# Optimization experiments

Hardware: AMD Instinct MI355X
Metric: run time of the kernel (lower is better)

The kernel has to match this reference:

```python
import jax, jax.numpy as jnp
import numpy as np

B, L = 8, 2500
VOCAB = 50000 + 2
E = 100          # dims[0], embed size
D = 128          # dims[1], conv filters
Y = 8921         # number of ICD9 labels
K = 9            # conv kernel size
PAD = K // 2


def setup_inputs() -> dict:
    key = jax.random.key(0)
    ks = jax.random.split(key, 8)
    x = jax.random.randint(ks[0], (B, L), 0, 50000)                      # token ids
    target = jax.random.uniform(ks[1], (B, Y), dtype=jnp.float32)        # soft binary targets
    emb_table = jax.random.normal(ks[2], (VOCAB, E), dtype=jnp.float32) * 0.1
    emb_table = emb_table.at[0].set(0.0)                                 # padding_idx=0
    # xavier-uniform-ish scales
    conv_w = jax.random.uniform(ks[3], (D, E, K), dtype=jnp.float32,
                                minval=-1.0, maxval=1.0) * np.sqrt(6.0 / (E * K + D * K))
    conv_b = jnp.zeros((D,), dtype=jnp.float32)
    U = jax.random.uniform(ks[4], (Y, D), dtype=jnp.float32,
                           minval=-1.0, maxval=1.0) * np.sqrt(6.0 / (Y + D))
    final_w = jax.random.uniform(ks[5], (Y, D), dtype=jnp.float32,
                                 minval=-1.0, maxval=1.0) * np.sqrt(6.0 / (Y + D))
    final_b = jnp.zeros((Y,), dtype=jnp.float32)
    return {"x": x, "target": target, "emb_table": emb_table,
            "conv_w": conv_w, "conv_b": conv_b, "U": U,
            "final_w": final_w, "final_b": final_b}


def _bce_with_logits(logits, target):
    # mean(max(z,0) - z*t + log(1+exp(-|z|)))
    return jnp.mean(jnp.maximum(logits, 0.0) - logits * target
                    + jnp.log1p(jnp.exp(-jnp.abs(logits))))


def reference(x, target, emb_table, conv_w, conv_b, U, final_w, final_b):
    e = emb_table[x]                                  # [B, L, E]  (dropout inactive at eval)
    # Conv1d over sequence, 'same' padding; conv_w is torch layout (Cout, Cin, K)
    h = jax.lax.conv_general_dilated(
        e, conv_w, window_strides=(1,), padding=[(PAD, PAD)],
        dimension_numbers=("NWC", "OIW", "NWC")) + conv_b
    h = jnp.tanh(h)                                   # [B, L, D]
    # Label-wise attention: scores [B, Y, L], softmax over sequence dim
    scores = jnp.einsum("yd,bld->byl", U, h)
    alpha = jax.nn.softmax(scores, axis=2)            # [B, Y, L]
    m = jnp.einsum("byl,bld->byd", alpha, h)          # [B, Y, D]
    logits = jnp.einsum("yd,byd->by", final_w, m) + final_b   # [B, Y]
    loss = _bce_with_logits(logits, target)
    yhat = jax.nn.sigmoid(logits)
    return yhat, loss, alpha
```

## Files before the change

kernel.cpp:

```cpp
#include <hip/hip_runtime.h>
#include <math.h>

#define B 8
#define LSEQ 2500
#define EDIM 100
#define DDIM 128
#define YLAB 8921
#define KW 9
#define BYTOT (B*YLAB)
#define LP 2560
#define NLBS 20
#define NYB 70
#define NPB 140

typedef __attribute__((ext_vector_type(8))) short bf16x8;
typedef __attribute__((ext_vector_type(8))) unsigned short u16x8;
typedef __attribute__((ext_vector_type(4))) float f32x4;

__device__ __forceinline__ ushort f2bf(float f){
    union { float f; unsigned u; } v; v.f = f;
    unsigned r = v.u + 0x7FFFu + ((v.u >> 16) & 1u);
    return (ushort)(r >> 16);
}
__device__ __forceinline__ float bf2f(ushort u){
    union { unsigned u; float f; } v; v.u = ((unsigned)u) << 16;
    return v.f;
}

#define OFF_HB 0
#define OFF_HT 1310720
#define OFF_UB 2621440
#define OFF_PS 3192384
#define OFF_RI 4619744
#define OFF_LG 4691112
#define OFF_LSP 4762480
#define OFF_WT 4762608

#define NP1 (DDIM*EDIM*KW)
#define NP2 (YLAB*DDIM)
#define NP3 (B*DDIM*(LP-LSEQ))
#define NP4 (B*(LP-LSEQ)*DDIM)
__global__ __launch_bounds__(256) void k_prep(const float* __restrict__ w, const float* __restrict__ U,
                                              float* __restrict__ wT, ushort* __restrict__ Ub,
                                              ushort* __restrict__ hT, ushort* __restrict__ hb){
    int i = blockIdx.x * 256 + threadIdx.x;
    if (i < NP1) {
        int k = i % KW, e = (i / KW) % EDIM, d = i / (KW * EDIM);
        wT[(k * EDIM + e) * DDIM + d] = w[i];
    }
    int i2 = i - NP1;
    if (i2 >= 0 && i2 < NP2) Ub[i2] = f2bf(U[i2]);
    int i3 = i - NP1 - NP2;
    if (i3 >= 0 && i3 < NP3) {
        int c = i3 % (LP - LSEQ), bd = i3 / (LP - LSEQ);
        hT[(size_t)bd * LP + LSEQ + c] = 0;
    }
    int i4 = i - NP1 - NP2 - NP3;
    if (i4 >= 0 && i4 < NP4) {
        int b = i4 / ((LP - LSEQ) * DDIM);
        int r = i4 % ((LP - LSEQ) * DDIM);
        int l = LSEQ + r / DDIM, d = r % DDIM;
        hb[((size_t)b * LP + l) * DDIM + d] = 0;
    }
}

#define CTL 20
__global__ __launch_bounds__(256) void k_conv(const int* __restrict__ x, const float* __restrict__ emb,
                                              const float* __restrict__ wT, const float* __restrict__ bias,
                                              ushort* __restrict__ hb, ushort* __restrict__ hT) {
    __shared__ float se[EDIM * 32];
    __shared__ ushort hstage[DDIM][CTL + 2];
    int blk = blockIdx.x;
    int b = blk / (LSEQ / CTL);
    int l0 = (blk % (LSEQ / CTL)) * CTL;
    int tid = threadIdx.x;
    for (int i = tid; i < (CTL + 8) * EDIM; i += 256) {
        int row = i / EDIM, e = i - row * EDIM;
        int l = l0 + row - 4;
        float v = 0.f;
        if (l >= 0 && l < LSEQ) {
            int tok = x[b * LSEQ + l];
            v = emb[(size_t)tok * EDIM + e];
        }
        se[e * 32 + row] = v;
    }
    __syncthreads();
    int d = tid & 127;
    int g = tid >> 7;
    float bv = bias[d];
    float acc[10];
#pragma unroll
    for (int li = 0; li < 10; li++) acc[li] = bv;
    for (int e = 0; e < EDIM; e++) {
        float r[20];
#pragma unroll
        for (int t2 = 0; t2 < 10; t2++) {
            float2 rr = *(const float2*)&se[e * 32 + g * 10 + 2 * t2];
            r[2 * t2] = rr.x; r[2 * t2 + 1] = rr.y;
        }
#pragma unroll
        for (int k = 0; k < KW; k++) {
            float wv = wT[(k * EDIM + e) * DDIM + d];
#pragma unroll
            for (int li = 0; li < 10; li++) acc[li] += r[li + k] * wv;
        }
    }
#pragma unroll
    for (int li = 0; li < 10; li++) {
        int l = l0 + g * 10 + li;
        ushort u = f2bf(tanhf(acc[li]));
        hb[((size_t)b * LP + l) * DDIM + d] = u;
        hstage[d][g * 10 + li] = u;
    }
    __syncthreads();
    int d2 = tid >> 1, half = tid & 1;
    size_t base = ((size_t)b * DDIM + d2) * LP + l0 + half * 10;
#pragma unroll
    for (int q = 0; q < 10; q++) hT[base + q] = hstage[d2][half * 10 + q];
}

__global__ __launch_bounds__(256) void k_sums(const ushort* __restrict__ hb, const ushort* __restrict__ Ub,
                                              float* __restrict__ psum) {
    int wg = blockIdx.x;
    int b = wg & 7;
    int r = wg >> 3;
    int lblk = r % NLBS, yblk = r / NLBS;
    int l0 = lblk * 128, y0 = yblk * 128;
    int tid = threadIdx.x, w = tid >> 6, lane = tid & 63, g = lane >> 4, ln = lane & 15;
    int h = w >> 1, lh = w & 1;
    int y0w = y0 + h * 64;
    bf16x8 zf = {0, 0, 0, 0, 0, 0, 0, 0};
    bf16x8 au[4][4];
    bool vya[4];
#pragma unroll
    for (int yf = 0; yf < 4; yf++) {
        int ya = y0w + yf * 16 + ln;
        vya[yf] = ya < YLAB;
        const ushort* Ap = Ub + (size_t)(vya[yf] ? ya : 0) * DDIM + g * 8;
#pragma unroll
        for (int kk = 0; kk < 4; kk++) au[yf][kk] = vya[yf] ? *(const bf16x8*)(Ap + kk * 32) : zf;
    }
    f32x4 zero4 = {0.f, 0.f, 0.f, 0.f};
    const ushort* hbB = hb + (size_t)b * LP * DDIM;
    float ts[4][4] = {};
#pragma unroll
    for (int lt = 0; lt < 2; lt++) {
        int lw = l0 + (lt * 2 + lh) * 32;
        f32x4 acc[4][2];
#pragma unroll
        for (int yf = 0; yf < 4; yf++) { acc[yf][0] = zero4; acc[yf][1] = zero4; }
#pragma unroll
        for (int kk = 0; kk < 4; kk++) {
            bf16x8 bv0 = *(const bf16x8*)(hbB + (size_t)(lw + ln) * DDIM + kk * 32 + g * 8);
            bf16x8 bv1 = *(const bf16x8*)(hbB + (size_t)(lw + 16 + ln) * DDIM + kk * 32 + g * 8);
#pragma unroll
            for (int yf = 0; yf < 4; yf++) {
                acc[yf][0] = __builtin_amdgcn_mfma_f32_16x16x32_bf16(au[yf][kk], bv0, acc[yf][0], 0, 0, 0);
                acc[yf][1] = __builtin_amdgcn_mfma_f32_16x16x32_bf16(au[yf][kk], bv1, acc[yf][1], 0, 0, 0);
            }
        }
#pragma unroll
        for (int yf = 0; yf < 4; yf++)
#pragma unroll
            for (int fl = 0; fl < 2; fl++)
#pragma unroll
                for (int j = 0; j < 4; j++) {
                    int y = y0w + yf * 16 + g * 4 + j;
                    int l = lw + fl * 16 + ln;
                    bool v = (y < YLAB) && (l < LSEQ);
                    ts[yf][j] += v ? __expf(acc[yf][fl][j]) : 0.f;
                }
    }
#pragma unroll
    for (int yf = 0; yf < 4; yf++)
#pragma unroll
        for (int j = 0; j < 4; j++) {
            float t = ts[yf][j];
            t += __shfl_xor(t, 1, 64); t += __shfl_xor(t, 2, 64);
            t += __shfl_xor(t, 4, 64); t += __shfl_xor(t, 8, 64);
            ts[yf][j] = t;
        }
    __shared__ float psl[2][128];
    if (ln == 0) {
#pragma unroll
        for (int yf = 0; yf < 4; yf++)
#pragma unroll
            for (int j = 0; j < 4; j++)
                psl[lh][h * 64 + yf * 16 + g * 4 + j] = ts[yf][j];
    }
    __syncthreads();
    if (tid < 128) {
        int y = y0 + tid;
        if (y < YLAB) psum[(size_t)lblk * BYTOT + b * YLAB + y] = psl[0][tid] + psl[1][tid];
    }
}

__global__ __launch_bounds__(256) void k_rinv(const float* __restrict__ psum, float* __restrict__ rinv) {
    int i = blockIdx.x * 256 + threadIdx.x;
    if (i >= BYTOT) return;
    float s = 0.f;
#pragma unroll
    for (int j = 0; j < NLBS; j++) s += psum[(size_t)j * BYTOT + i];
    rinv[i] = 1.f / s;
}

__global__ __launch_bounds__(256) void k_pool(const ushort* __restrict__ hb, const ushort* __restrict__ hT,
                                              const ushort* __restrict__ Ub, const float* __restrict__ rinv,
                                              const float* __restrict__ fw, const float* __restrict__ fb,
                                              float* __restrict__ alpha, float* __restrict__ yhat,
                                              float* __restrict__ logits) {
    __shared__ ushort hbs[32 * 128];
    __shared__ ushort hts[128 * 40];
    __shared__ ushort et[4][16 * 44];
    int wg = blockIdx.x;
    int b = wg & 7;
    int y0 = (wg >> 3) * 64;
    int tid = threadIdx.x, w = tid >> 6, lane = tid & 63, g = lane >> 4, ln = lane & 15;
    int y0w = y0 + w * 16;
    bf16x8 zf = {0, 0, 0, 0, 0, 0, 0, 0};
    int ya = y0w + ln;
    bool vya = ya < YLAB;
    const ushort* Ap = Ub + (size_t)(vya ? ya : 0) * DDIM + g * 8;
    bf16x8 au[4];
#pragma unroll
    for (int kk = 0; kk < 4; kk++) au[kk] = vya ? *(const bf16x8*)(Ap + kk * 32) : zf;
    float rvl = vya ? rinv[b * YLAB + ya] : 0.f;
    f32x4 zero4 = {0.f, 0.f, 0.f, 0.f};
    f32x4 accm[8];
#pragma unroll
    for (int fd = 0; fd < 8; fd++) accm[fd] = zero4;

    int s0 = tid, s1 = tid + 256;
    const ushort* hbB = hb + (size_t)b * LP * DDIM;
    const ushort* htB = hT + (size_t)b * DDIM * LP;
    int l_a = s0 >> 4, sg_a = s0 & 15, l_b = s1 >> 4, sg_b = s1 & 15;
    int d_a = s0 >> 2, q_a = s0 & 3, d_b = s1 >> 2, q_b = s1 & 3;
    int wsg_a = sg_a ^ (l_a & 7), wsg_b = sg_b ^ (l_b & 7);
    u16x8 rhb0, rhb1, rht0, rht1;
    rhb0 = *(const u16x8*)(hbB + (size_t)l_a * DDIM + sg_a * 8);
    rhb1 = *(const u16x8*)(hbB + (size_t)l_b * DDIM + sg_b * 8);
    rht0 = *(const u16x8*)(htB + (size_t)d_a * LP + q_a * 8);
    rht1 = *(const u16x8*)(htB + (size_t)d_b * LP + q_b * 8);

    float* aB = alpha + (size_t)b * YLAB * LSEQ;

    for (int l0 = 0; l0 < LP; l0 += 32) {
        *(u16x8*)&hbs[l_a * DDIM + wsg_a * 8] = rhb0;
        *(u16x8*)&hbs[l_b * DDIM + wsg_b * 8] = rhb1;
        *(u16x8*)&hts[d_a * 40 + q_a * 8] = rht0;
        *(u16x8*)&hts[d_b * 40 + q_b * 8] = rht1;
        __syncthreads();
        if (l0 + 32 < LP) {
            int ln0 = l0 + 32;
            rhb0 = *(const u16x8*)(hbB + (size_t)(ln0 + l_a) * DDIM + sg_a * 8);
            rhb1 = *(const u16x8*)(hbB + (size_t)(ln0 + l_b) * DDIM + sg_b * 8);
            rht0 = *(const u16x8*)(htB + (size_t)d_a * LP + ln0 + q_a * 8);
            rht1 = *(const u16x8*)(htB + (size_t)d_b * LP + ln0 + q_b * 8);
        }
        f32x4 sc[2];
        sc[0] = zero4; sc[1] = zero4;
#pragma unroll
        for (int kk = 0; kk < 4; kk++)
#pragma unroll
            for (int fl = 0; fl < 2; fl++) {
                int lrow = fl * 16 + ln;
                int slotr = (kk * 4 + g) ^ (lrow & 7);
                bf16x8 bv = *(const bf16x8*)&hbs[lrow * DDIM + slotr * 8];
                sc[fl] = __builtin_amdgcn_mfma_f32_16x16x32_bf16(bv, au[kk], sc[fl], 0, 0, 0);
            }
#pragma unroll
        for (int fl = 0; fl < 2; fl++) {
            float an0 = __expf(sc[fl][0]) * rvl;
            float an1 = __expf(sc[fl][1]) * rvl;
            float an2 = __expf(sc[fl][2]) * rvl;
            float an3 = __expf(sc[fl][3]) * rvl;
            unsigned long long pk =
                (unsigned long long)f2bf(an0) | ((unsigned long long)f2bf(an1) << 16) |
                ((unsigned long long)f2bf(an2) << 32) | ((unsigned long long)f2bf(an3) << 48);
            *(unsigned long long*)&et[w][ln * 44 + fl * 16 + g * 4] = pk;
        }
        bf16x8 af = *(const bf16x8*)&et[w][ln * 44 + g * 8];
#pragma unroll
        for (int fd = 0; fd < 8; fd++) {
            bf16x8 bt = *(const bf16x8*)&hts[(fd * 16 + ln) * 40 + g * 8];
            accm[fd] = __builtin_amdgcn_mfma_f32_16x16x32_bf16(af, bt, accm[fd], 0, 0, 0);
        }
        if (l0 + 32 <= LSEQ) {
#pragma unroll
            for (int i = 0; i < 8; i++) {
                int r = i * 2 + (lane >> 5);
                int c = lane & 31;
                int y = y0w + r;
                if (y < YLAB) aB[(size_t)y * LSEQ + l0 + c] = bf2f(et[w][r * 44 + c]);
            }
        } else if (l0 < LSEQ) {
#pragma unroll
            for (int i = 0; i < 8; i++) {
                int r = i * 2 + (lane >> 5);
                int c = lane & 31;
                int y = y0w + r;
                int l = l0 + c;
                if (y < YLAB && l < LSEQ) aB[(size_t)y * LSEQ + l] = bf2f(et[w][r * 44 + c]);
            }
        }
        __syncthreads();
    }
    float lp[4] = {0.f, 0.f, 0.f, 0.f};
#pragma unroll
    for (int j = 0; j < 4; j++) {
        int yr = y0w + g * 4 + j;
        bool vr = yr < YLAB;
#pragma unroll
        for (int fd = 0; fd < 8; fd++) {
            float fwv = vr ? fw[(size_t)yr * DDIM + fd * 16 + ln] : 0.f;
            lp[j] += accm[fd][j] * fwv;
        }
    }
#pragma unroll
    for (int j = 0; j < 4; j++) {
        float t = lp[j];
        t += __shfl_xor(t, 1, 64); t += __shfl_xor(t, 2, 64);
        t += __shfl_xor(t, 4, 64); t += __shfl_xor(t, 8, 64);
        lp[j] = t;
    }
    if (ln == 0) {
#pragma unroll
        for (int j = 0; j < 4; j++) {
            int yr = y0w + g * 4 + j;
            if (yr < YLAB) {
                float lg = lp[j] + fb[yr];
                int idx = b * YLAB + yr;
                logits[idx] = lg;
                yhat[idx] = 1.f / (1.f + expf(-lg));
            }
        }
    }
}

__global__ __launch_bounds__(256) void k_loss1(const float* __restrict__ logits, const float* __restrict__ target,
                                               float* __restrict__ partials) {
    int tid = threadIdx.x;
    int base = blockIdx.x * 1024;
    float sum = 0.f;
#pragma unroll
    for (int q = 0; q < 4; q++) {
        int i = base + q * 256 + tid;
        if (i < BYTOT) {
            float z = logits[i], t = target[i];
            sum += fmaxf(z, 0.f) - z * t + log1pf(expf(-fabsf(z)));
        }
    }
    for (int o = 32; o > 0; o >>= 1) sum += __shfl_down(sum, o, 64);
    __shared__ float red[4];
    if ((tid & 63) == 0) red[tid >> 6] = sum;
    __syncthreads();
    if (tid == 0) partials[blockIdx.x] = red[0] + red[1] + red[2] + red[3];
}

__global__ __launch_bounds__(128) void k_loss2(const float* __restrict__ partials, float* __restrict__ out_loss) {
    int tid = threadIdx.x;
    float s = (tid < 70) ? partials[tid] : 0.f;
    for (int o = 32; o > 0; o >>= 1) s += __shfl_down(s, o, 64);
    __shared__ float red[2];
    if ((tid & 63) == 0) red[tid >> 6] = s;
    __syncthreads();
    if (tid == 0) out_loss[0] = (red[0] + red[1]) / (float)BYTOT;
}

extern "C" void kernel_launch(void* const* d_in, const int* in_sizes, int n_in,
                              void* d_out, int out_size, void* d_ws, size_t ws_size,
                              hipStream_t stream) {
    const int* x = (const int*)d_in[0];
    const float* target = (const float*)d_in[1];
    const float* emb = (const float*)d_in[2];
    const float* conv_w = (const float*)d_in[3];
    const float* conv_b = (const float*)d_in[4];
    const float* U = (const float*)d_in[5];
    const float* fw = (const float*)d_in[6];
    const float* fb = (const float*)d_in[7];

    float* out = (float*)d_out;
    float* yhat = out;
    float* loss = out + BYTOT;
    float* alpha = out + BYTOT + 1;

    float* ws = (float*)d_ws;
    ushort* hb = (ushort*)(ws + OFF_HB);
    ushort* hT = (ushort*)(ws + OFF_HT);
    ushort* Ub = (ushort*)(ws + OFF_UB);
    float* psum = ws + OFF_PS;
    float* rinv = ws + OFF_RI;
    float* logits = ws + OFF_LG;
    float* lpart = ws + OFF_LSP;
    float* wT = ws + OFF_WT;

    k_prep<<<(NP1 + NP2 + NP3 + NP4 + 255) / 256, 256, 0, stream>>>(conv_w, U, wT, Ub, hT, hb);
    k_conv<<<B * (LSEQ / CTL), 256, 0, stream>>>(x, emb, wT, conv_b, hb, hT);
    k_sums<<<NYB * NLBS * B, 256, 0, stream>>>(hb, Ub, psum);
    k_rinv<<<(BYTOT + 255) / 256, 256, 0, stream>>>(psum, rinv);
    k_pool<<<NPB * B, 256, 0, stream>>>(hb, hT, Ub, rinv, fw, fb, alpha, yhat, logits);
    k_loss1<<<70, 256, 0, stream>>>(logits, target, lpart);
    k_loss2<<<1, 128, 0, stream>>>(lpart, loss);
}
```

Before: 634.3 us.

## Materialize unnormalized exp scores in k_sums and reuse them in k_pool

k_sums now writes the bf16 exp(score) values to a workspace buffer of shape [B*Y, LP] alongside the partial sums. k_pool no longer recomputes the U·h scores. It streams these stored exponentials, scales them by the reciprocal sum to produce alpha, and applies the normalization to the logits after the weighted pooling. This removes the second score GEMM and the exp work, and drops the LDS staging and barriers. The cost is writing and re-reading a roughly 365 MB bf16 intermediate, so the kernel leans much harder on memory bandwidth. Alpha is also now rounded from the unnormalized bf16 exponential and then scaled.

```diff
diff --git a/kernel.cpp b/kernel.cpp
--- a/kernel.cpp
+++ b/kernel.cpp
@@ -12,9 +12,9 @@
 #define NLBS 20
 #define NYB 70
 #define NPB 140
+#define LPOOL 2528
 
 typedef __attribute__((ext_vector_type(8))) short bf16x8;
-typedef __attribute__((ext_vector_type(8))) unsigned short u16x8;
 typedef __attribute__((ext_vector_type(4))) float f32x4;
 
 __device__ __forceinline__ ushort f2bf(float f){
@@ -35,6 +35,7 @@
 #define OFF_LG 4691112
 #define OFF_LSP 4762480
 #define OFF_WT 4762608
+#define OFF_EB 4877808
 
 #define NP1 (DDIM*EDIM*KW)
 #define NP2 (YLAB*DDIM)
@@ -120,78 +121,74 @@
 }
 
 __global__ __launch_bounds__(256) void k_sums(const ushort* __restrict__ hb, const ushort* __restrict__ Ub,
-                                              float* __restrict__ psum) {
+                                              float* __restrict__ psum, ushort* __restrict__ ebuf) {
     int wg = blockIdx.x;
     int b = wg & 7;
     int r = wg >> 3;
     int lblk = r % NLBS, yblk = r / NLBS;
     int l0 = lblk * 128, y0 = yblk * 128;
     int tid = threadIdx.x, w = tid >> 6, lane = tid & 63, g = lane >> 4, ln = lane & 15;
-    int h = w >> 1, lh = w & 1;
-    int y0w = y0 + h * 64;
+    int y0w = y0 + w * 32;
     bf16x8 zf = {0, 0, 0, 0, 0, 0, 0, 0};
-    bf16x8 au[4][4];
-    bool vya[4];
-#pragma unroll
-    for (int yf = 0; yf < 4; yf++) {
-        int ya = y0w + yf * 16 + ln;
-        vya[yf] = ya < YLAB;
-        const ushort* Ap = Ub + (size_t)(vya[yf] ? ya : 0) * DDIM + g * 8;
-#pragma unroll
-        for (int kk = 0; kk < 4; kk++) au[yf][kk] = vya[yf] ? *(const bf16x8*)(Ap + kk * 32) : zf;
-    }
+    bf16x8 au[2][4];
+    bool vya[2];
+    int yv[2];
+#pragma unroll
+    for (int yg = 0; yg < 2; yg++) {
+        int y = y0w + yg * 16 + ln;
+        vya[yg] = y < YLAB;
+        yv[yg] = vya[yg] ? y : 0;
+        const ushort* Ap = Ub + (size_t)yv[yg] * DDIM + g * 8;
+#pragma unroll
+        for (int kk = 0; kk < 4; kk++) au[yg][kk] = vya[yg] ? *(const bf16x8*)(Ap + kk * 32) : zf;
+    }
+    const ushort* hbB = hb + (size_t)b * LP * DDIM;
     f32x4 zero4 = {0.f, 0.f, 0.f, 0.f};
-    const ushort* hbB = hb + (size_t)b * LP * DDIM;
-    float ts[4][4] = {};
-#pragma unroll
-    for (int lt = 0; lt < 2; lt++) {
-        int lw = l0 + (lt * 2 + lh) * 32;
-        f32x4 acc[4][2];
-#pragma unroll
-        for (int yf = 0; yf < 4; yf++) { acc[yf][0] = zero4; acc[yf][1] = zero4; }
-#pragma unroll
-        for (int kk = 0; kk < 4; kk++) {
-            bf16x8 bv0 = *(const bf16x8*)(hbB + (size_t)(lw + ln) * DDIM + kk * 32 + g * 8);
-            bf16x8 bv1 = *(const bf16x8*)(hbB + (size_t)(lw + 16 + ln) * DDIM + kk * 32 + g * 8);
-#pragma unroll
-            for (int yf = 0; yf < 4; yf++) {
-                acc[yf][0] = __builtin_amdgcn_mfma_f32_16x16x32_bf16(au[yf][kk], bv0, acc[yf][0], 0, 0, 0);
-                acc[yf][1] = __builtin_amdgcn_mfma_f32_16x16x32_bf16(au[yf][kk], bv1, acc[yf][1], 0, 0, 0);
+    float ts[2] = {0.f, 0.f};
+#pragma unroll
+    for (int lt = 0; lt < 4; lt++) {
+        int lw = l0 + lt * 32;
+        bf16x8 a[2][4];
+#pragma unroll
+        for (int fl = 0; fl < 2; fl++)
+#pragma unroll
+            for (int kk = 0; kk < 4; kk++)
+                a[fl][kk] = *(const bf16x8*)(hbB + (size_t)(lw + fl * 16 + ln) * DDIM + kk * 32 + g * 8);
+        f32x4 sc[2][2];
+        sc[0][0] = zero4; sc[0][1] = zero4; sc[1][0] = zero4; sc[1][1] = zero4;
+#pragma unroll
+        for (int kk = 0; kk < 4; kk++)
+#pragma unroll
+            for (int fl = 0; fl < 2; fl++) {
+                sc[0][fl] = __builtin_amdgcn_mfma_f32_16x16x32_bf16(a[fl][kk], au[0][kk], sc[0][fl], 0, 0, 0);
+                sc[1][fl] = __builtin_amdgcn_mfma_f32_16x16x32_bf16(a[fl][kk], au[1][kk], sc[1][fl], 0, 0, 0);
             }
-        }
-#pragma unroll
-        for (int yf = 0; yf < 4; yf++)
-#pragma unroll
-            for (int fl = 0; fl < 2; fl++)
-#pragma unroll
-                for (int j = 0; j < 4; j++) {
-                    int y = y0w + yf * 16 + g * 4 + j;
-                    int l = lw + fl * 16 + ln;
-                    bool v = (y < YLAB) && (l < LSEQ);
-                    ts[yf][j] += v ? __expf(acc[yf][fl][j]) : 0.f;
-                }
-    }
-#pragma unroll
-    for (int yf = 0; yf < 4; yf++)
-#pragma unroll
-        for (int j = 0; j < 4; j++) {
-            float t = ts[yf][j];
-            t += __shfl_xor(t, 1, 64); t += __shfl_xor(t, 2, 64);
-            t += __shfl_xor(t, 4, 64); t += __shfl_xor(t, 8, 64);
-            ts[yf][j] = t;
-        }
-    __shared__ float psl[2][128];
-    if (ln == 0) {
-#pragma unroll
-        for (int yf = 0; yf < 4; yf++)
-#pragma unroll
-            for (int j = 0; j < 4; j++)
-                psl[lh][h * 64 + yf * 16 + g * 4 + j] = ts[yf][j];
-    }
-    __syncthreads();
-    if (tid < 128) {
-        int y = y0 + tid;
-        if (y < YLAB) psum[(size_t)lblk * BYTOT + b * YLAB + y] = psl[0][tid] + psl[1][tid];
+#pragma unroll
+        for (int yg = 0; yg < 2; yg++) {
+            size_t ebrow = (size_t)(b * YLAB + yv[yg]) * LP;
+#pragma unroll
+            for (int fl = 0; fl < 2; fl++) {
+                float e0, e1, e2, e3;
+                int lb = lw + fl * 16 + g * 4;
+                e0 = (lb + 0 < LSEQ) ? __expf(sc[yg][fl][0]) : 0.f;
+                e1 = (lb + 1 < LSEQ) ? __expf(sc[yg][fl][1]) : 0.f;
+                e2 = (lb + 2 < LSEQ) ? __expf(sc[yg][fl][2]) : 0.f;
+                e3 = (lb + 3 < LSEQ) ? __expf(sc[yg][fl][3]) : 0.f;
+                ts[yg] += (e0 + e1) + (e2 + e3);
+                unsigned long long pk =
+                    (unsigned long long)f2bf(e0) | ((unsigned long long)f2bf(e1) << 16) |
+                    ((unsigned long long)f2bf(e2) << 32) | ((unsigned long long)f2bf(e3) << 48);
+                if (vya[yg]) *(unsigned long long*)&ebuf[ebrow + lb] = pk;
+            }
+        }
+    }
+#pragma unroll
+    for (int yg = 0; yg < 2; yg++) {
+        float t = ts[yg];
+        t += __shfl_xor(t, 16, 64);
+        t += __shfl_xor(t, 32, 64);
+        if (g == 0 && vya[yg])
+            psum[(size_t)lblk * BYTOT + b * YLAB + y0w + yg * 16 + ln] = t;
     }
 }
 
@@ -204,106 +201,56 @@
     rinv[i] = 1.f / s;
 }
 
-__global__ __launch_bounds__(256) void k_pool(const ushort* __restrict__ hb, const ushort* __restrict__ hT,
-                                              const ushort* __restrict__ Ub, const float* __restrict__ rinv,
-                                              const float* __restrict__ fw, const float* __restrict__ fb,
-                                              float* __restrict__ alpha, float* __restrict__ yhat,
-                                              float* __restrict__ logits) {
-    __shared__ ushort hbs[32 * 128];
-    __shared__ ushort hts[128 * 40];
-    __shared__ ushort et[4][16 * 44];
+__global__ __launch_bounds__(256) void k_pool(const ushort* __restrict__ ebuf, const ushort* __restrict__ hT,
+                                              const float* __restrict__ rinv, const float* __restrict__ fw,
+                                              const float* __restrict__ fb, float* __restrict__ alpha,
+                                              float* __restrict__ yhat, float* __restrict__ logits) {
     int wg = blockIdx.x;
     int b = wg & 7;
     int y0 = (wg >> 3) * 64;
     int tid = threadIdx.x, w = tid >> 6, lane = tid & 63, g = lane >> 4, ln = lane & 15;
     int y0w = y0 + w * 16;
-    bf16x8 zf = {0, 0, 0, 0, 0, 0, 0, 0};
     int ya = y0w + ln;
     bool vya = ya < YLAB;
-    const ushort* Ap = Ub + (size_t)(vya ? ya : 0) * DDIM + g * 8;
-    bf16x8 au[4];
-#pragma unroll
-    for (int kk = 0; kk < 4; kk++) au[kk] = vya ? *(const bf16x8*)(Ap + kk * 32) : zf;
+    int yc = vya ? ya : 0;
     float rvl = vya ? rinv[b * YLAB + ya] : 0.f;
+    const ushort* eR = ebuf + (size_t)(b * YLAB + yc) * LP + g * 8;
+    const ushort* htB = hT + (size_t)b * DDIM * LP + g * 8;
+    float* aRow = alpha + (size_t)(b * YLAB + yc) * LSEQ;
+    bf16x8 zf = {0, 0, 0, 0, 0, 0, 0, 0};
     f32x4 zero4 = {0.f, 0.f, 0.f, 0.f};
     f32x4 accm[8];
 #pragma unroll
     for (int fd = 0; fd < 8; fd++) accm[fd] = zero4;
 
-    int s0 = tid, s1 = tid + 256;
-    const ushort* hbB = hb + (size_t)b * LP * DDIM;
-    const ushort* htB = hT + (size_t)b * DDIM * LP;
-    int l_a = s0 >> 4, sg_a = s0 & 15, l_b = s1 >> 4, sg_b = s1 & 15;
-    int d_a = s0 >> 2, q_a = s0 & 3, d_b = s1 >> 2, q_b = s1 & 3;
-    int wsg_a = sg_a ^ (l_a & 7), wsg_b = sg_b ^ (l_b & 7);
-    u16x8 rhb0, rhb1, rht0, rht1;
-    rhb0 = *(const u16x8*)(hbB + (size_t)l_a * DDIM + sg_a * 8);
-    rhb1 = *(const u16x8*)(hbB + (size_t)l_b * DDIM + sg_b * 8);
-    rht0 = *(const u16x8*)(htB + (size_t)d_a * LP + q_a * 8);
-    rht1 = *(const u16x8*)(htB + (size_t)d_b * LP + q_b * 8);
-
-    float* aB = alpha + (size_t)b * YLAB * LSEQ;
-
-    for (int l0 = 0; l0 < LP; l0 += 32) {
-        *(u16x8*)&hbs[l_a * DDIM + wsg_a * 8] = rhb0;
-        *(u16x8*)&hbs[l_b * DDIM + wsg_b * 8] = rhb1;
-        *(u16x8*)&hts[d_a * 40 + q_a * 8] = rht0;
-        *(u16x8*)&hts[d_b * 40 + q_b * 8] = rht1;
-        __syncthreads();
-        if (l0 + 32 < LP) {
-            int ln0 = l0 + 32;
-            rhb0 = *(const u16x8*)(hbB + (size_t)(ln0 + l_a) * DDIM + sg_a * 8);
-            rhb1 = *(const u16x8*)(hbB + (size_t)(ln0 + l_b) * DDIM + sg_b * 8);
-            rht0 = *(const u16x8*)(htB + (size_t)d_a * LP + ln0 + q_a * 8);
-            rht1 = *(const u16x8*)(htB + (size_t)d_b * LP + ln0 + q_b * 8);
-        }
-        f32x4 sc[2];
-        sc[0] = zero4; sc[1] = zero4;
-#pragma unroll
-        for (int kk = 0; kk < 4; kk++)
-#pragma unroll
-            for (int fl = 0; fl < 2; fl++) {
-                int lrow = fl * 16 + ln;
-                int slotr = (kk * 4 + g) ^ (lrow & 7);
-                bf16x8 bv = *(const bf16x8*)&hbs[lrow * DDIM + slotr * 8];
-                sc[fl] = __builtin_amdgcn_mfma_f32_16x16x32_bf16(bv, au[kk], sc[fl], 0, 0, 0);
+    for (int l0 = 0; l0 < LPOOL; l0 += 32) {
+        bf16x8 ar = *(const bf16x8*)(eR + l0);
+        bf16x8 af = vya ? ar : zf;
+#pragma unroll
+        for (int fd = 0; fd < 8; fd++) {
+            bf16x8 bt = *(const bf16x8*)(htB + (size_t)(fd * 16 + ln) * LP + l0);
+            accm[fd] = __builtin_amdgcn_mfma_f32_16x16x32_bf16(af, bt, accm[fd], 0, 0, 0);
+        }
+        if (vya) {
+            float f[8];
+#pragma unroll
+            for (int q = 0; q < 8; q++) f[q] = bf2f((ushort)ar[q]) * rvl;
+            int lb = l0 + g * 8;
+            if (lb + 8 <= LSEQ) {
+                *(float4*)&aRow[lb] = make_float4(f[0], f[1], f[2], f[3]);
+                *(float4*)&aRow[lb + 4] = make_float4(f[4], f[5], f[6], f[7]);
+            } else {
+#pragma unroll
+                for (int q = 0; q < 8; q++)
+                    if (lb + q < LSEQ) aRow[lb + q] = f[q];
             }
-#pragma unroll
-        for (int fl = 0; fl < 2; fl++) {
-            float an0 = __expf(sc[fl][0]) * rvl;
-            float an1 = __expf(sc[fl][1]) * rvl;
-            float an2 = __expf(sc[fl][2]) * rvl;
-            float an3 = __expf(sc[fl][3]) * rvl;
-            unsigned long long pk =
-                (unsigned long long)f2bf(an0) | ((unsigned long long)f2bf(an1) << 16) |
-                ((unsigned long long)f2bf(an2) << 32) | ((unsigned long long)f2bf(an3) << 48);
-            *(unsigned long long*)&et[w][ln * 44 + fl * 16 + g * 4] = pk;
-        }
-        bf16x8 af = *(const bf16x8*)&et[w][ln * 44 + g * 8];
-#pragma unroll
-        for (int fd = 0; fd < 8; fd++) {
-            bf16x8 bt = *(const bf16x8*)&hts[(fd * 16 + ln) * 40 + g * 8];
-            accm[fd] = __builtin_amdgcn_mfma_f32_16x16x32_bf16(af, bt, accm[fd], 0, 0, 0);
-        }
-        if (l0 + 32 <= LSEQ) {
-#pragma unroll
-            for (int i = 0; i < 8; i++) {
-                int r = i * 2 + (lane >> 5);
-                int c = lane & 31;
-                int y = y0w + r;
-                if (y < YLAB) aB[(size_t)y * LSEQ + l0 + c] = bf2f(et[w][r * 44 + c]);
-            }
-        } else if (l0 < LSEQ) {
-#pragma unroll
-            for (int i = 0; i < 8; i++) {
-                int r = i * 2 + (lane >> 5);
-                int c = lane & 31;
-                int y = y0w + r;
-                int l = l0 + c;
-                if (y < YLAB && l < LSEQ) aB[(size_t)y * LSEQ + l] = bf2f(et[w][r * 44 + c]);
-            }
-        }
-        __syncthreads();
+        }
+    }
+    float rin4[4];
+#pragma unroll
+    for (int j = 0; j < 4; j++) {
+        int yr = y0w + g * 4 + j;
+        rin4[j] = (yr < YLAB) ? rinv[b * YLAB + yr] : 0.f;
     }
     float lp[4] = {0.f, 0.f, 0.f, 0.f};
 #pragma unroll
@@ -321,7 +268,7 @@
         float t = lp[j];
         t += __shfl_xor(t, 1, 64); t += __shfl_xor(t, 2, 64);
         t += __shfl_xor(t, 4, 64); t += __shfl_xor(t, 8, 64);
-        lp[j] = t;
+        lp[j] = t * rin4[j];
     }
     if (ln == 0) {
 #pragma unroll
@@ -393,12 +340,13 @@
     float* logits = ws + OFF_LG;
     float* lpart = ws + OFF_LSP;
     float* wT = ws + OFF_WT;
+    ushort* ebuf = (ushort*)(ws + OFF_EB);
 
     k_prep<<<(NP1 + NP2 + NP3 + NP4 + 255) / 256, 256, 0, stream>>>(conv_w, U, wT, Ub, hT, hb);
     k_conv<<<B * (LSEQ / CTL), 256, 0, stream>>>(x, emb, wT, conv_b, hb, hT);
-    k_sums<<<NYB * NLBS * B, 256, 0, stream>>>(hb, Ub, psum);
+    k_sums<<<NYB * NLBS * B, 256, 0, stream>>>(hb, Ub, psum, ebuf);
     k_rinv<<<(BYTOT + 255) / 256, 256, 0, stream>>>(psum, rinv);
-    k_pool<<<NPB * B, 256, 0, stream>>>(hb, hT, Ub, rinv, fw, fb, alpha, yhat, logits);
+    k_pool<<<NPB * B, 256, 0, stream>>>(ebuf, hT, rinv, fw, fb, alpha, yhat, logits);
     k_loss1<<<70, 256, 0, stream>>>(logits, target, lpart);
     k_loss2<<<1, 128, 0, stream>>>(lpart, loss);
 }
```

Result: slower. 1.049 ms (+65.4%).

## Fold softmax normalizer reduction into pool kernel and retile k_sums per-wave

Applied to the files above, without the earlier changes.

Removes the separate k_rinv launch. Each pool workgroup now sums the partial exp-sums for its 64 labels into shared memory and reads the reciprocal after the first barrier. k_sums is retiled so each wave owns 32 labels across all 128 positions, with h as the MFMA A operand, which leaves the label sums in lane-local registers. That cuts the shuffle, shared-memory and barrier reduction down to two cross-group shuffles. The cost is redundant psum reads across workgroups that share a label block, and a different register and load pattern in k_sums.

```diff
diff --git a/kernel.cpp b/kernel.cpp
--- a/kernel.cpp
+++ b/kernel.cpp
@@ -31,7 +31,6 @@
 #define OFF_HT 1310720
 #define OFF_UB 2621440
 #define OFF_PS 3192384
-#define OFF_RI 4619744
 #define OFF_LG 4691112
 #define OFF_LSP 4762480
 #define OFF_WT 4762608
@@ -127,91 +126,68 @@
     int lblk = r % NLBS, yblk = r / NLBS;
     int l0 = lblk * 128, y0 = yblk * 128;
     int tid = threadIdx.x, w = tid >> 6, lane = tid & 63, g = lane >> 4, ln = lane & 15;
-    int h = w >> 1, lh = w & 1;
-    int y0w = y0 + h * 64;
+    int y0w = y0 + w * 32;
     bf16x8 zf = {0, 0, 0, 0, 0, 0, 0, 0};
-    bf16x8 au[4][4];
-    bool vya[4];
-#pragma unroll
-    for (int yf = 0; yf < 4; yf++) {
-        int ya = y0w + yf * 16 + ln;
-        vya[yf] = ya < YLAB;
-        const ushort* Ap = Ub + (size_t)(vya[yf] ? ya : 0) * DDIM + g * 8;
-#pragma unroll
-        for (int kk = 0; kk < 4; kk++) au[yf][kk] = vya[yf] ? *(const bf16x8*)(Ap + kk * 32) : zf;
-    }
+    bf16x8 au[2][4];
+    bool vya[2];
+#pragma unroll
+    for (int yg = 0; yg < 2; yg++) {
+        int y = y0w + yg * 16 + ln;
+        vya[yg] = y < YLAB;
+        const ushort* Ap = Ub + (size_t)(vya[yg] ? y : 0) * DDIM + g * 8;
+#pragma unroll
+        for (int kk = 0; kk < 4; kk++) au[yg][kk] = vya[yg] ? *(const bf16x8*)(Ap + kk * 32) : zf;
+    }
+    const ushort* hbB = hb + (size_t)b * LP * DDIM;
     f32x4 zero4 = {0.f, 0.f, 0.f, 0.f};
-    const ushort* hbB = hb + (size_t)b * LP * DDIM;
-    float ts[4][4] = {};
-#pragma unroll
-    for (int lt = 0; lt < 2; lt++) {
-        int lw = l0 + (lt * 2 + lh) * 32;
-        f32x4 acc[4][2];
-#pragma unroll
-        for (int yf = 0; yf < 4; yf++) { acc[yf][0] = zero4; acc[yf][1] = zero4; }
-#pragma unroll
-        for (int kk = 0; kk < 4; kk++) {
-            bf16x8 bv0 = *(const bf16x8*)(hbB + (size_t)(lw + ln) * DDIM + kk * 32 + g * 8);
-            bf16x8 bv1 = *(const bf16x8*)(hbB + (size_t)(lw + 16 + ln) * DDIM + kk * 32 + g * 8);
-#pragma unroll
-            for (int yf = 0; yf < 4; yf++) {
-                acc[yf][0] = __builtin_amdgcn_mfma_f32_16x16x32_bf16(au[yf][kk], bv0, acc[yf][0], 0, 0, 0);
-                acc[yf][1] = __builtin_amdgcn_mfma_f32_16x16x32_bf16(au[yf][kk], bv1, acc[yf][1], 0, 0, 0);
-            }
-        }
-#pragma unroll
-        for (int yf = 0; yf < 4; yf++)
-#pragma unroll
-            for (int fl = 0; fl < 2; fl++)
-#pragma unroll
-                for (int j = 0; j < 4; j++) {
-                    int y = y0w + yf * 16 + g * 4 + j;
-                    int l = lw + fl * 16 + ln;
-                    bool v = (y < YLAB) && (l < LSEQ);
-                    ts[yf][j] += v ? __expf(acc[yf][fl][j]) : 0.f;
-                }
-    }
-#pragma unroll
-    for (int yf = 0; yf < 4; yf++)
-#pragma unroll
-        for (int j = 0; j < 4; j++) {
-            float t = ts[yf][j];
-            t += __shfl_xor(t, 1, 64); t += __shfl_xor(t, 2, 64);
-            t += __shfl_xor(t, 4, 64); t += __shfl_xor(t, 8, 64);
-            ts[yf][j] = t;
-        }
-    __shared__ float psl[2][128];
-    if (ln == 0) {
-#pragma unroll
-        for (int yf = 0; yf < 4; yf++)
-#pragma unroll
-            for (int j = 0; j < 4; j++)
-                psl[lh][h * 64 + yf * 16 + g * 4 + j] = ts[yf][j];
-    }
-    __syncthreads();
-    if (tid < 128) {
-        int y = y0 + tid;
-        if (y < YLAB) psum[(size_t)lblk * BYTOT + b * YLAB + y] = psl[0][tid] + psl[1][tid];
-    }
-}
-
-__global__ __launch_bounds__(256) void k_rinv(const float* __restrict__ psum, float* __restrict__ rinv) {
-    int i = blockIdx.x * 256 + threadIdx.x;
-    if (i >= BYTOT) return;
-    float s = 0.f;
-#pragma unroll
-    for (int j = 0; j < NLBS; j++) s += psum[(size_t)j * BYTOT + i];
-    rinv[i] = 1.f / s;
+    float ts[2] = {0.f, 0.f};
+#pragma unroll
+    for (int lt = 0; lt < 4; lt++) {
+        int lw = l0 + lt * 32;
+        bf16x8 a[2][4];
+#pragma unroll
+        for (int fl = 0; fl < 2; fl++)
+#pragma unroll
+            for (int kk = 0; kk < 4; kk++)
+                a[fl][kk] = *(const bf16x8*)(hbB + (size_t)(lw + fl * 16 + ln) * DDIM + kk * 32 + g * 8);
+        f32x4 sc[2][2];
+        sc[0][0] = zero4; sc[0][1] = zero4; sc[1][0] = zero4; sc[1][1] = zero4;
+#pragma unroll
+        for (int kk = 0; kk < 4; kk++)
+#pragma unroll
+            for (int fl = 0; fl < 2; fl++) {
+                sc[0][fl] = __builtin_amdgcn_mfma_f32_16x16x32_bf16(a[fl][kk], au[0][kk], sc[0][fl], 0, 0, 0);
+                sc[1][fl] = __builtin_amdgcn_mfma_f32_16x16x32_bf16(a[fl][kk], au[1][kk], sc[1][fl], 0, 0, 0);
+            }
+#pragma unroll
+        for (int yg = 0; yg < 2; yg++)
+#pragma unroll
+            for (int fl = 0; fl < 2; fl++) {
+                int lb = lw + fl * 16 + g * 4;
+#pragma unroll
+                for (int j = 0; j < 4; j++)
+                    ts[yg] += (lb + j < LSEQ) ? __expf(sc[yg][fl][j]) : 0.f;
+            }
+    }
+#pragma unroll
+    for (int yg = 0; yg < 2; yg++) {
+        float t = ts[yg];
+        t += __shfl_xor(t, 16, 64);
+        t += __shfl_xor(t, 32, 64);
+        if (g == 0 && vya[yg])
+            psum[(size_t)lblk * BYTOT + b * YLAB + y0w + yg * 16 + ln] = t;
+    }
 }
 
 __global__ __launch_bounds__(256) void k_pool(const ushort* __restrict__ hb, const ushort* __restrict__ hT,
-                                              const ushort* __restrict__ Ub, const float* __restrict__ rinv,
+                                              const ushort* __restrict__ Ub, const float* __restrict__ psum,
                                               const float* __restrict__ fw, const float* __restrict__ fb,
                                               float* __restrict__ alpha, float* __restrict__ yhat,
                                               float* __restrict__ logits) {
     __shared__ ushort hbs[32 * 128];
     __shared__ ushort hts[128 * 40];
     __shared__ ushort et[4][16 * 44];
+    __shared__ float rinvS[64];
     int wg = blockIdx.x;
     int b = wg & 7;
     int y0 = (wg >> 3) * 64;
@@ -224,7 +200,16 @@
     bf16x8 au[4];
 #pragma unroll
     for (int kk = 0; kk < 4; kk++) au[kk] = vya ? *(const bf16x8*)(Ap + kk * 32) : zf;
-    float rvl = vya ? rinv[b * YLAB + ya] : 0.f;
+    if (tid < 64) {
+        int y = y0 + tid;
+        float s = 1.f;
+        if (y < YLAB) {
+            s = 0.f;
+#pragma unroll
+            for (int j = 0; j < NLBS; j++) s += psum[(size_t)j * BYTOT + b * YLAB + y];
+        }
+        rinvS[tid] = 1.f / s;
+    }
     f32x4 zero4 = {0.f, 0.f, 0.f, 0.f};
     f32x4 accm[8];
 #pragma unroll
@@ -243,6 +228,8 @@
     rht1 = *(const u16x8*)(htB + (size_t)d_b * LP + q_b * 8);
 
     float* aB = alpha + (size_t)b * YLAB * LSEQ;
+    float rvl = 0.f;
+    bool first = true;
 
     for (int l0 = 0; l0 < LP; l0 += 32) {
         *(u16x8*)&hbs[l_a * DDIM + wsg_a * 8] = rhb0;
@@ -250,6 +237,7 @@
         *(u16x8*)&hts[d_a * 40 + q_a * 8] = rht0;
         *(u16x8*)&hts[d_b * 40 + q_b * 8] = rht1;
         __syncthreads();
+        if (first) { rvl = vya ? rinvS[w * 16 + ln] : 0.f; first = false; }
         if (l0 + 32 < LP) {
             int ln0 = l0 + 32;
             rhb0 = *(const u16x8*)(hbB + (size_t)(ln0 + l_a) * DDIM + sg_a * 8);
@@ -389,7 +377,6 @@
     ushort* hT = (ushort*)(ws + OFF_HT);
     ushort* Ub = (ushort*)(ws + OFF_UB);
     float* psum = ws + OFF_PS;
-    float* rinv = ws + OFF_RI;
     float* logits = ws + OFF_LG;
     float* lpart = ws + OFF_LSP;
     float* wT = ws + OFF_WT;
@@ -397,8 +384,7 @@
     k_prep<<<(NP1 + NP2 + NP3 + NP4 + 255) / 256, 256, 0, stream>>>(conv_w, U, wT, Ub, hT, hb);
     k_conv<<<B * (LSEQ / CTL), 256, 0, stream>>>(x, emb, wT, conv_b, hb, hT);
     k_sums<<<NYB * NLBS * B, 256, 0, stream>>>(hb, Ub, psum);
-    k_rinv<<<(BYTOT + 255) / 256, 256, 0, stream>>>(psum, rinv);
-    k_pool<<<NPB * B, 256, 0, stream>>>(hb, hT, Ub, rinv, fw, fb, alpha, yhat, logits);
+    k_pool<<<NPB * B, 256, 0, stream>>>(hb, hT, Ub, psum, fw, fb, alpha, yhat, logits);
     k_loss1<<<70, 256, 0, stream>>>(logits, target, lpart);
     k_loss2<<<1, 128, 0, stream>>>(lpart, loss);
 }
```

Result: slower. 664.9 us (+4.8%).
